# Kernel optimization log

Hardware: AMD Instinct MI355X
Metric: run time of the kernel (lower is better)

The kernel has to match this reference:

```python
import jax, jax.numpy as jnp
import numpy as np

N, L, D = 2, 1024, 4544
H, DKV = 71, 64
ROPE_BASE = 10000.0


def _rope_tables(seq_len, head_dim, dtype):
    inv_freq = 1.0 / (ROPE_BASE ** (jnp.arange(0, head_dim, 2, dtype=jnp.float32) / head_dim))
    t = jnp.arange(seq_len, dtype=jnp.float32)
    freqs = jnp.outer(t, inv_freq)               # [L, Dkv/2]
    emb = jnp.concatenate([freqs, freqs], -1)    # [L, Dkv]
    return jnp.cos(emb).astype(dtype), jnp.sin(emb).astype(dtype)


def _apply_rotary(x, cos, sin):
    # x: [..., L, Dkv]; cos/sin: [L, Dkv] broadcast
    left, right = jnp.split(x, 2, axis=-1)
    rotated = jnp.concatenate([-right, left], axis=-1)
    return x * cos + rotated * sin


def setup_inputs() -> dict:
    key = jax.random.key(0)
    k1, k2, k3 = jax.random.split(key, 3)
    hidden_states = jax.random.normal(k1, (N, L, D), dtype=jnp.float32)
    w_qkv = jax.random.normal(k2, (D + 2 * DKV, D), dtype=jnp.float32) * (1.0 / np.sqrt(D))
    w_dense = jax.random.normal(k3, (D, D), dtype=jnp.float32) * (1.0 / np.sqrt(D))
    return {"hidden_states": hidden_states, "w_qkv": w_qkv, "w_dense": w_dense}


def reference(hidden_states, w_qkv, w_dense):
    n, l, d = hidden_states.shape
    # fused QKV projection -> [N, L, H+2, Dkv]
    fused = (hidden_states @ w_qkv.T).reshape(n, l, H + 2, DKV)
    q = fused[:, :, :-2, :]          # [N, L, H, Dkv]
    k = fused[:, :, -2, :]           # [N, L, Dkv] (single MQA kv head)
    v = fused[:, :, -1, :]           # [N, L, Dkv]

    cos, sin = _rope_tables(l, DKV, hidden_states.dtype)
    q = _apply_rotary(q, cos[:, None, :], sin[:, None, :])   # broadcast over heads
    k = _apply_rotary(k, cos, sin)

    scale = 1.0 / np.sqrt(DKV)
    # scores: [N, H, Lq, Lk]; kv head broadcast across all H query heads
    scores = jnp.einsum('nqhd,nkd->nhqk', q, k) * scale
    causal = jnp.tril(jnp.ones((l, l), dtype=bool))
    scores = jnp.where(causal, scores, jnp.finfo(scores.dtype).min)
    attn = jax.nn.softmax(scores, axis=-1)
    out = jnp.einsum('nhqk,nkd->nqhd', attn, v)              # [N, L, H, Dkv]
    out = out.reshape(n, l, H * DKV)
    return out @ w_dense.T
```

## Files before the change

kernel.cpp:

```cpp
#include <hip/hip_runtime.h>

typedef unsigned short u16;
typedef __attribute__((ext_vector_type(8))) short short8;
typedef __attribute__((ext_vector_type(4))) float floatx4;

__device__ __forceinline__ u16 f2bf(float f) {
    union { float f; unsigned int u; } v;
    v.f = f;
    unsigned int u = v.u;
    return (u16)((u + 0x7FFFu + ((u >> 16) & 1u)) >> 16);
}

__device__ __forceinline__ void cvt8_f32_bf16(const float* __restrict__ p, u16* dst) {
    const float4 x = *(const float4*)p;
    const float4 y = *(const float4*)(p + 4);
    short8 s;
    s[0] = (short)f2bf(x.x); s[1] = (short)f2bf(x.y);
    s[2] = (short)f2bf(x.z); s[3] = (short)f2bf(x.w);
    s[4] = (short)f2bf(y.x); s[5] = (short)f2bf(y.y);
    s[6] = (short)f2bf(y.z); s[7] = (short)f2bf(y.w);
    *(short8*)dst = s;
}

__device__ __forceinline__ void gld_lds16(const u16* g, u16* l) {
    __builtin_amdgcn_global_load_lds(
        (const __attribute__((address_space(1))) void*)g,
        (__attribute__((address_space(3))) void*)l,
        16, 0, 0);
}

__global__ __launch_bounds__(256) void cvt3_kernel(
    const float* __restrict__ a, u16* __restrict__ oa, long na,
    const float* __restrict__ b, u16* __restrict__ ob, long nb,
    const float* __restrict__ c, u16* __restrict__ oc, long nc) {
    const float* in; u16* out; long n;
    if (blockIdx.y == 0)      { in = a; out = oa; n = na; }
    else if (blockIdx.y == 1) { in = b; out = ob; n = nb; }
    else                      { in = c; out = oc; n = nc; }
    const long i = ((long)blockIdx.x * 256 + threadIdx.x) * 8;
    if (i >= n) return;
    cvt8_f32_bf16(in + i, out + i);
}

__global__ __launch_bounds__(256) void gemm_qkv_bf(const u16* __restrict__ A,
                                                   const u16* __restrict__ B,
                                                   u16* __restrict__ qb,
                                                   u16* __restrict__ kb,
                                                   u16* __restrict__ vt,
                                                   int M, int N, int K) {
    __shared__ __align__(16) u16 a_lds[128 * 32];
    __shared__ __align__(16) u16 b_lds[128 * 32];
    const int t    = threadIdx.x;
    const int lane = t & 63;
    const int w    = t >> 6;
    const int quad = lane >> 4;
    const int l16  = lane & 15;
    const int m0 = blockIdx.y * 128;
    const int n0 = blockIdx.x * 128;
    const int wm = (w >> 1) * 64;
    const int wn = (w & 1) * 64;

    const int srow = t >> 2;
    const int scol = (t & 3) * 8;
    const u16* Ap0 = A + (long)(m0 + srow) * K + scol;
    const u16* Ap1 = A + (long)(m0 + 64 + srow) * K + scol;
    int bn0 = n0 + srow;      if (bn0 >= N) bn0 = N - 1;
    int bn1 = n0 + 64 + srow; if (bn1 >= N) bn1 = N - 1;
    const u16* Bp0 = B + (long)bn0 * K + scol;
    const u16* Bp1 = B + (long)bn1 * K + scol;

    u16* as0 = a_lds + srow * 32 + scol;
    u16* as1 = a_lds + (64 + srow) * 32 + scol;
    u16* bs0 = b_lds + srow * 32 + scol;
    u16* bs1 = b_lds + (64 + srow) * 32 + scol;

    floatx4 acc[4][4];
    const floatx4 zf4 = {0.f, 0.f, 0.f, 0.f};
#pragma unroll
    for (int i = 0; i < 4; i++)
#pragma unroll
        for (int j = 0; j < 4; j++) acc[i][j] = zf4;

    for (int k0 = 0; k0 < K; k0 += 32) {
        gld_lds16(Ap0 + k0, as0);
        gld_lds16(Ap1 + k0, as1);
        gld_lds16(Bp0 + k0, bs0);
        gld_lds16(Bp1 + k0, bs1);
        __syncthreads();
        short8 af[4], bfr[4];
#pragma unroll
        for (int i = 0; i < 4; i++)
            af[i] = *(const short8*)(a_lds + (wm + i * 16 + l16) * 32 + quad * 8);
#pragma unroll
        for (int j = 0; j < 4; j++)
            bfr[j] = *(const short8*)(b_lds + (wn + j * 16 + l16) * 32 + quad * 8);
#pragma unroll
        for (int i = 0; i < 4; i++)
#pragma unroll
            for (int j = 0; j < 4; j++)
                acc[i][j] = __builtin_amdgcn_mfma_f32_16x16x32_bf16(af[i], bfr[j], acc[i][j], 0, 0, 0);
        __syncthreads();
    }

#pragma unroll
    for (int j = 0; j < 4; j++) {
        const int c = n0 + wn + j * 16 + l16;
        if (c >= N) continue;
        const int hh = c >> 6;
        const int d  = c & 63;
        float inv = 0.f;
        if (hh < 72) inv = expf((float)(2 * (d & 31)) * (-0.14391156831212787f));
#pragma unroll
        for (int i = 0; i < 4; i++) {
#pragma unroll
            for (int r = 0; r < 4; r++) {
                const int row = m0 + wm + i * 16 + quad * 4 + r;
                const int tn = row >> 10;
                const int tl = row & 1023;
                float val = acc[i][j][r];
                if (hh < 72) {
                    float sv, cv;
                    sincosf((float)tl * inv, &sv, &cv);
                    const float pacc = acc[i][j ^ 2][r];
                    val = val * cv + ((d < 32) ? -pacc : pacc) * sv;
                }
                if (hh < 71) {
                    qb[((long)((tn * 71 + hh) * 1024 + tl)) * 64 + d] = f2bf(val * 0.125f);
                } else if (hh == 71) {
                    kb[((long)(tn * 1024 + tl)) * 64 + d] = f2bf(val);
                } else {
                    vt[((long)(tn * 64 + d)) * 1024 + tl] = f2bf(val);
                }
            }
        }
    }
}

__global__ __launch_bounds__(256) void gemm_dense_bf(const u16* __restrict__ A,
                                                     const u16* __restrict__ B,
                                                     float* __restrict__ C,
                                                     int M, int N, int K) {
    __shared__ __align__(16) u16 a_lds[128 * 32];
    __shared__ __align__(16) u16 b_lds[128 * 32];
    const int t    = threadIdx.x;
    const int lane = t & 63;
    const int w    = t >> 6;
    const int quad = lane >> 4;
    const int l16  = lane & 15;
    const int m0 = blockIdx.y * 128;
    const int n0 = blockIdx.x * 128;
    const int wm = (w >> 1) * 64;
    const int wn = (w & 1) * 64;

    const int srow = t >> 2;
    const int scol = (t & 3) * 8;
    const u16* Ap0 = A + (long)(m0 + srow) * K + scol;
    const u16* Ap1 = A + (long)(m0 + 64 + srow) * K + scol;
    int bn0 = n0 + srow;      if (bn0 >= N) bn0 = N - 1;
    int bn1 = n0 + 64 + srow; if (bn1 >= N) bn1 = N - 1;
    const u16* Bp0 = B + (long)bn0 * K + scol;
    const u16* Bp1 = B + (long)bn1 * K + scol;

    u16* as0 = a_lds + srow * 32 + scol;
    u16* as1 = a_lds + (64 + srow) * 32 + scol;
    u16* bs0 = b_lds + srow * 32 + scol;
    u16* bs1 = b_lds + (64 + srow) * 32 + scol;

    floatx4 acc[4][4];
    const floatx4 zf4 = {0.f, 0.f, 0.f, 0.f};
#pragma unroll
    for (int i = 0; i < 4; i++)
#pragma unroll
        for (int j = 0; j < 4; j++) acc[i][j] = zf4;

    for (int k0 = 0; k0 < K; k0 += 32) {
        gld_lds16(Ap0 + k0, as0);
        gld_lds16(Ap1 + k0, as1);
        gld_lds16(Bp0 + k0, bs0);
        gld_lds16(Bp1 + k0, bs1);
        __syncthreads();
        short8 af[4], bfr[4];
#pragma unroll
        for (int i = 0; i < 4; i++)
            af[i] = *(const short8*)(a_lds + (wm + i * 16 + l16) * 32 + quad * 8);
#pragma unroll
        for (int j = 0; j < 4; j++)
            bfr[j] = *(const short8*)(b_lds + (wn + j * 16 + l16) * 32 + quad * 8);
#pragma unroll
        for (int i = 0; i < 4; i++)
#pragma unroll
            for (int j = 0; j < 4; j++)
                acc[i][j] = __builtin_amdgcn_mfma_f32_16x16x32_bf16(af[i], bfr[j], acc[i][j], 0, 0, 0);
        __syncthreads();
    }

#pragma unroll
    for (int i = 0; i < 4; i++) {
#pragma unroll
        for (int j = 0; j < 4; j++) {
            const int col = n0 + wn + j * 16 + l16;
            if (col < N) {
#pragma unroll
                for (int r = 0; r < 4; r++) {
                    const int row = m0 + wm + i * 16 + quad * 4 + r;
                    C[(long)row * N + col] = acc[i][j][r];
                }
            }
        }
    }
}

__global__ __launch_bounds__(256) void attn_kernel2(const u16* __restrict__ qb,
                                                    const u16* __restrict__ kb,
                                                    const u16* __restrict__ vt,
                                                    u16* __restrict__ ao) {
    __shared__ __align__(16) u16 k_lds[2][64 * 72];
    __shared__ __align__(16) u16 v_lds[2][64 * 72];
    __shared__ __align__(16) u16 p_lds[4][16 * 72];
    const int qt2 = blockIdx.x;
    const int h   = blockIdx.y;
    const int n   = blockIdx.z;
    const int t    = threadIdx.x;
    const int w    = t >> 6;
    const int lane = t & 63;
    const int quad = lane >> 4;
    const int l16  = lane & 15;
    const int Q0 = qt2 * 128;

    short8 aq[2][2];
#pragma unroll
    for (int mf = 0; mf < 2; mf++) {
        const u16* qrow = qb +
            ((long)((n * 71 + h) * 1024 + Q0 + 64 * mf + w * 16 + l16)) * 64;
        aq[mf][0] = *(const short8*)(qrow + quad * 8);
        aq[mf][1] = *(const short8*)(qrow + 32 + quad * 8);
    }

    floatx4 o[2][4];
    float lst[2][4];
    const floatx4 zf4 = {0.f, 0.f, 0.f, 0.f};
#pragma unroll
    for (int mf = 0; mf < 2; mf++) {
#pragma unroll
        for (int i = 0; i < 4; i++) { o[mf][i] = zf4; lst[mf][i] = 0.f; }
    }

    const int srow = t >> 2;
    const int scol = (t & 3) * 16;
    const u16* kb_n = kb + (long)n * 1024 * 64;
    const u16* vt_n = vt + (long)n * 64 * 1024;
    u16* pw = p_lds[w];

    const int ktend = 2 * qt2 + 2;

    auto stage = [&](int kt, int b) {
        const u16* krow = kb_n + (long)(kt * 64 + srow) * 64 + scol;
        *(uint4*)(k_lds[b] + srow * 72 + scol)     = *(const uint4*)(krow);
        *(uint4*)(k_lds[b] + srow * 72 + scol + 8) = *(const uint4*)(krow + 8);
        const u16* vrow = vt_n + (long)srow * 1024 + kt * 64 + scol;
        *(uint4*)(v_lds[b] + srow * 72 + scol)     = *(const uint4*)(vrow);
        *(uint4*)(v_lds[b] + srow * 72 + scol + 8) = *(const uint4*)(vrow + 8);
    };

    stage(0, 0);
    for (int kt = 0; kt < ktend; kt++) {
        const int buf = kt & 1;
        __syncthreads();
        if (kt + 1 < ktend) stage(kt + 1, 1 - buf);

#pragma unroll
        for (int mf = 0; mf < 2; mf++) {
            if (mf == 0 && kt == 2 * qt2 + 1) continue;
            floatx4 s[4];
#pragma unroll
            for (int sub = 0; sub < 4; sub++) {
                const short8 b0 = *(const short8*)(k_lds[buf] + (sub * 16 + l16) * 72 + quad * 8);
                const short8 b1 = *(const short8*)(k_lds[buf] + (sub * 16 + l16) * 72 + 32 + quad * 8);
                floatx4 z = zf4;
                z = __builtin_amdgcn_mfma_f32_16x16x32_bf16(aq[mf][0], b0, z, 0, 0, 0);
                z = __builtin_amdgcn_mfma_f32_16x16x32_bf16(aq[mf][1], b1, z, 0, 0, 0);
                s[sub] = z;
            }
            const bool diag = (kt == 2 * qt2 + mf);
            const int rowb = Q0 + 64 * mf + w * 16 + quad * 4;
#pragma unroll
            for (int sub = 0; sub < 4; sub++) {
                const int key = kt * 64 + sub * 16 + l16;
#pragma unroll
                for (int r = 0; r < 4; r++) {
                    float p = __expf(s[sub][r]);
                    if (diag && key > rowb + r) p = 0.f;
                    lst[mf][r] += p;
                    pw[(quad * 4 + r) * 72 + sub * 16 + l16] = f2bf(p);
                }
            }
            const short8 ap0 = *(const short8*)(pw + l16 * 72 + quad * 8);
            const short8 ap1 = *(const short8*)(pw + l16 * 72 + 32 + quad * 8);
#pragma unroll
            for (int dch = 0; dch < 4; dch++) {
                const short8 bv0 = *(const short8*)(v_lds[buf] + (dch * 16 + l16) * 72 + quad * 8);
                const short8 bv1 = *(const short8*)(v_lds[buf] + (dch * 16 + l16) * 72 + 32 + quad * 8);
                o[mf][dch] = __builtin_amdgcn_mfma_f32_16x16x32_bf16(ap0, bv0, o[mf][dch], 0, 0, 0);
                o[mf][dch] = __builtin_amdgcn_mfma_f32_16x16x32_bf16(ap1, bv1, o[mf][dch], 0, 0, 0);
            }
        }
    }

    float lsum[2][4];
#pragma unroll
    for (int mf = 0; mf < 2; mf++) {
#pragma unroll
        for (int r = 0; r < 4; r++) {
            float v = lst[mf][r];
#pragma unroll
            for (int mk = 1; mk < 16; mk <<= 1) v += __shfl_xor(v, mk, 64);
            lsum[mf][r] = v;
        }
    }
#pragma unroll
    for (int mf = 0; mf < 2; mf++) {
#pragma unroll
        for (int dch = 0; dch < 4; dch++) {
#pragma unroll
            for (int r = 0; r < 4; r++) {
                const float val = o[mf][dch][r] / lsum[mf][r];
                const int row = n * 1024 + Q0 + 64 * mf + w * 16 + quad * 4 + r;
                const int col = h * 64 + dch * 16 + l16;
                ao[(long)row * 4544 + col] = f2bf(val);
            }
        }
    }
}

__global__ __launch_bounds__(256) void gemm_qkv_f32(const float* __restrict__ A,
                                                    const float* __restrict__ B,
                                                    u16* __restrict__ qb,
                                                    u16* __restrict__ kb,
                                                    u16* __restrict__ vt,
                                                    int M, int N, int K) {
    __shared__ __align__(16) u16 a_lds[128 * 32];
    __shared__ __align__(16) u16 b_lds[128 * 32];
    const int t    = threadIdx.x;
    const int lane = t & 63;
    const int w    = t >> 6;
    const int quad = lane >> 4;
    const int l16  = lane & 15;
    const int m0 = blockIdx.y * 128;
    const int n0 = blockIdx.x * 128;
    const int wm = (w >> 1) * 64;
    const int wn = (w & 1) * 64;
    const int srow = t >> 2;
    const int scol = (t & 3) * 8;
    const float* Ap0 = A + (long)(m0 + srow) * K + scol;
    const float* Ap1 = A + (long)(m0 + 64 + srow) * K + scol;
    int bn0 = n0 + srow;      if (bn0 >= N) bn0 = N - 1;
    int bn1 = n0 + 64 + srow; if (bn1 >= N) bn1 = N - 1;
    const float* Bp0 = B + (long)bn0 * K + scol;
    const float* Bp1 = B + (long)bn1 * K + scol;
    u16* as0 = a_lds + srow * 32 + scol;
    u16* as1 = a_lds + (64 + srow) * 32 + scol;
    u16* bs0 = b_lds + srow * 32 + scol;
    u16* bs1 = b_lds + (64 + srow) * 32 + scol;
    floatx4 acc[4][4];
    const floatx4 zf4 = {0.f, 0.f, 0.f, 0.f};
#pragma unroll
    for (int i = 0; i < 4; i++)
#pragma unroll
        for (int j = 0; j < 4; j++) acc[i][j] = zf4;
    for (int k0 = 0; k0 < K; k0 += 32) {
        cvt8_f32_bf16(Ap0 + k0, as0);
        cvt8_f32_bf16(Ap1 + k0, as1);
        cvt8_f32_bf16(Bp0 + k0, bs0);
        cvt8_f32_bf16(Bp1 + k0, bs1);
        __syncthreads();
        short8 af[4], bfr[4];
#pragma unroll
        for (int i = 0; i < 4; i++)
            af[i] = *(const short8*)(a_lds + (wm + i * 16 + l16) * 32 + quad * 8);
#pragma unroll
        for (int j = 0; j < 4; j++)
            bfr[j] = *(const short8*)(b_lds + (wn + j * 16 + l16) * 32 + quad * 8);
#pragma unroll
        for (int i = 0; i < 4; i++)
#pragma unroll
            for (int j = 0; j < 4; j++)
                acc[i][j] = __builtin_amdgcn_mfma_f32_16x16x32_bf16(af[i], bfr[j], acc[i][j], 0, 0, 0);
        __syncthreads();
    }
#pragma unroll
    for (int j = 0; j < 4; j++) {
        const int c = n0 + wn + j * 16 + l16;
        if (c >= N) continue;
        const int hh = c >> 6;
        const int d  = c & 63;
        float inv = 0.f;
        if (hh < 72) inv = expf((float)(2 * (d & 31)) * (-0.14391156831212787f));
#pragma unroll
        for (int i = 0; i < 4; i++) {
#pragma unroll
            for (int r = 0; r < 4; r++) {
                const int row = m0 + wm + i * 16 + quad * 4 + r;
                const int tn = row >> 10;
                const int tl = row & 1023;
                float val = acc[i][j][r];
                if (hh < 72) {
                    float sv, cv;
                    sincosf((float)tl * inv, &sv, &cv);
                    const float pacc = acc[i][j ^ 2][r];
                    val = val * cv + ((d < 32) ? -pacc : pacc) * sv;
                }
                if (hh < 71) {
                    qb[((long)((tn * 71 + hh) * 1024 + tl)) * 64 + d] = f2bf(val * 0.125f);
                } else if (hh == 71) {
                    kb[((long)(tn * 1024 + tl)) * 64 + d] = f2bf(val);
                } else {
                    vt[((long)(tn * 64 + d)) * 1024 + tl] = f2bf(val);
                }
            }
        }
    }
}

__global__ __launch_bounds__(256) void gemm_dense_f32(const u16* __restrict__ A,
                                                      const float* __restrict__ B,
                                                      float* __restrict__ C,
                                                      int M, int N, int K) {
    __shared__ __align__(16) u16 a_lds[128 * 32];
    __shared__ __align__(16) u16 b_lds[128 * 32];
    const int t    = threadIdx.x;
    const int lane = t & 63;
    const int w    = t >> 6;
    const int quad = lane >> 4;
    const int l16  = lane & 15;
    const int m0 = blockIdx.y * 128;
    const int n0 = blockIdx.x * 128;
    const int wm = (w >> 1) * 64;
    const int wn = (w & 1) * 64;
    const int srow = t >> 2;
    const int scol = (t & 3) * 8;
    const u16* Ap0 = A + (long)(m0 + srow) * K + scol;
    const u16* Ap1 = A + (long)(m0 + 64 + srow) * K + scol;
    int bn0 = n0 + srow;      if (bn0 >= N) bn0 = N - 1;
    int bn1 = n0 + 64 + srow; if (bn1 >= N) bn1 = N - 1;
    const float* Bp0 = B + (long)bn0 * K + scol;
    const float* Bp1 = B + (long)bn1 * K + scol;
    u16* as0 = a_lds + srow * 32 + scol;
    u16* as1 = a_lds + (64 + srow) * 32 + scol;
    u16* bs0 = b_lds + srow * 32 + scol;
    u16* bs1 = b_lds + (64 + srow) * 32 + scol;
    floatx4 acc[4][4];
    const floatx4 zf4 = {0.f, 0.f, 0.f, 0.f};
#pragma unroll
    for (int i = 0; i < 4; i++)
#pragma unroll
        for (int j = 0; j < 4; j++) acc[i][j] = zf4;
    for (int k0 = 0; k0 < K; k0 += 32) {
        *(uint4*)as0 = *(const uint4*)(Ap0 + k0);
        *(uint4*)as1 = *(const uint4*)(Ap1 + k0);
        cvt8_f32_bf16(Bp0 + k0, bs0);
        cvt8_f32_bf16(Bp1 + k0, bs1);
        __syncthreads();
        short8 af[4], bfr[4];
#pragma unroll
        for (int i = 0; i < 4; i++)
            af[i] = *(const short8*)(a_lds + (wm + i * 16 + l16) * 32 + quad * 8);
#pragma unroll
        for (int j = 0; j < 4; j++)
            bfr[j] = *(const short8*)(b_lds + (wn + j * 16 + l16) * 32 + quad * 8);
#pragma unroll
        for (int i = 0; i < 4; i++)
#pragma unroll
            for (int j = 0; j < 4; j++)
                acc[i][j] = __builtin_amdgcn_mfma_f32_16x16x32_bf16(af[i], bfr[j], acc[i][j], 0, 0, 0);
        __syncthreads();
    }
#pragma unroll
    for (int i = 0; i < 4; i++) {
#pragma unroll
        for (int j = 0; j < 4; j++) {
            const int col = n0 + wn + j * 16 + l16;
            if (col < N) {
#pragma unroll
                for (int r = 0; r < 4; r++) {
                    const int row = m0 + wm + i * 16 + quad * 4 + r;
                    C[(long)row * N + col] = acc[i][j][r];
                }
            }
        }
    }
}

extern "C" void kernel_launch(void* const* d_in, const int* in_sizes, int n_in,
                              void* d_out, int out_size, void* d_ws, size_t ws_size,
                              hipStream_t stream) {
    (void)in_sizes; (void)n_in; (void)out_size;
    const float* hidden  = (const float*)d_in[0];
    const float* w_qkv   = (const float*)d_in[1];
    const float* w_dense = (const float*)d_in[2];
    float* out = (float*)d_out;

    const long N_HID = (long)2048 * 4544;
    const long N_QKV = (long)4672 * 4544;
    const long N_DEN = (long)4544 * 4544;
    const long N_Q   = (long)2 * 71 * 1024 * 64;
    const long N_KV  = (long)2 * 1024 * 64;
    const long N_AO  = (long)2048 * 4544;

    const size_t needA = (size_t)(N_HID + N_QKV + N_DEN + N_Q + 2 * N_KV + N_AO) * 2;

    if (ws_size >= needA) {
        u16* hid_bf  = (u16*)d_ws;
        u16* wqkv_bf = hid_bf + N_HID;
        u16* wden_bf = wqkv_bf + N_QKV;
        u16* qbuf    = wden_bf + N_DEN;
        u16* kbuf    = qbuf + N_Q;
        u16* vtbuf   = kbuf + N_KV;
        u16* aout    = vtbuf + N_KV;

        cvt3_kernel<<<dim3(10366, 3), 256, 0, stream>>>(
            hidden, hid_bf, N_HID, w_qkv, wqkv_bf, N_QKV, w_dense, wden_bf, N_DEN);
        gemm_qkv_bf<<<dim3(37, 16), 256, 0, stream>>>(hid_bf, wqkv_bf,
                                                      qbuf, kbuf, vtbuf,
                                                      2048, 4672, 4544);
        attn_kernel2<<<dim3(8, 71, 2), 256, 0, stream>>>(qbuf, kbuf, vtbuf, aout);
        gemm_dense_bf<<<dim3(36, 16), 256, 0, stream>>>(aout, wden_bf, out,
                                                        2048, 4544, 4544);
    } else {
        u16* qbuf  = (u16*)d_ws;
        u16* kbuf  = qbuf + N_Q;
        u16* vtbuf = kbuf + N_KV;
        u16* aout  = vtbuf + N_KV;
        gemm_qkv_f32<<<dim3(37, 16), 256, 0, stream>>>(hidden, w_qkv,
                                                       qbuf, kbuf, vtbuf,
                                                       2048, 4672, 4544);
        attn_kernel2<<<dim3(8, 71, 2), 256, 0, stream>>>(qbuf, kbuf, vtbuf, aout);
        gemm_dense_f32<<<dim3(36, 16), 256, 0, stream>>>(aout, w_dense, out,
                                                         2048, 4544, 4544);
    }
}
```

Measured before the change: 616.5 us.

## Replace QKV and dense GEMMs with 256x256 8-wave pipelined double-buffered kernels

Both bf16 GEMMs move from 128x128 tiles with a single-buffered K=32 loop to 256x256 tiles run by 512 threads. Operands are double-buffered in LDS with K=64 steps and XOR-swizzled columns, and global-to-LDS loads are interleaved with MFMA phases using explicit barriers, waitcnt and setprio. Workgroup IDs are remapped across the 8 XCDs for cache locality. This aims to raise MFMA utilisation and hide load latency, at the cost of 128 KB of LDS per block and fewer blocks in the grid (152 and 144), which may leave some CUs idle.

```diff
diff --git a/kernel.cpp b/kernel.cpp
--- a/kernel.cpp
+++ b/kernel.cpp
@@ -42,86 +42,141 @@
     cvt8_f32_bf16(in + i, out + i);
 }
 
-__global__ __launch_bounds__(256) void gemm_qkv_bf(const u16* __restrict__ A,
-                                                   const u16* __restrict__ B,
-                                                   u16* __restrict__ qb,
-                                                   u16* __restrict__ kb,
-                                                   u16* __restrict__ vt,
-                                                   int M, int N, int K) {
-    __shared__ __align__(16) u16 a_lds[128 * 32];
-    __shared__ __align__(16) u16 b_lds[128 * 32];
-    const int t    = threadIdx.x;
-    const int lane = t & 63;
-    const int w    = t >> 6;
-    const int quad = lane >> 4;
-    const int l16  = lane & 15;
-    const int m0 = blockIdx.y * 128;
-    const int n0 = blockIdx.x * 128;
-    const int wm = (w >> 1) * 64;
-    const int wn = (w & 1) * 64;
-
-    const int srow = t >> 2;
-    const int scol = (t & 3) * 8;
-    const u16* Ap0 = A + (long)(m0 + srow) * K + scol;
-    const u16* Ap1 = A + (long)(m0 + 64 + srow) * K + scol;
-    int bn0 = n0 + srow;      if (bn0 >= N) bn0 = N - 1;
-    int bn1 = n0 + 64 + srow; if (bn1 >= N) bn1 = N - 1;
-    const u16* Bp0 = B + (long)bn0 * K + scol;
-    const u16* Bp1 = B + (long)bn1 * K + scol;
-
-    u16* as0 = a_lds + srow * 32 + scol;
-    u16* as1 = a_lds + (64 + srow) * 32 + scol;
-    u16* bs0 = b_lds + srow * 32 + scol;
-    u16* bs1 = b_lds + (64 + srow) * 32 + scol;
-
-    floatx4 acc[4][4];
-    const floatx4 zf4 = {0.f, 0.f, 0.f, 0.f};
-#pragma unroll
-    for (int i = 0; i < 4; i++)
-#pragma unroll
-        for (int j = 0; j < 4; j++) acc[i][j] = zf4;
-
-    for (int k0 = 0; k0 < K; k0 += 32) {
-        gld_lds16(Ap0 + k0, as0);
-        gld_lds16(Ap1 + k0, as1);
-        gld_lds16(Bp0 + k0, bs0);
-        gld_lds16(Bp1 + k0, bs1);
-        __syncthreads();
-        short8 af[4], bfr[4];
-#pragma unroll
-        for (int i = 0; i < 4; i++)
-            af[i] = *(const short8*)(a_lds + (wm + i * 16 + l16) * 32 + quad * 8);
-#pragma unroll
-        for (int j = 0; j < 4; j++)
-            bfr[j] = *(const short8*)(b_lds + (wn + j * 16 + l16) * 32 + quad * 8);
-#pragma unroll
-        for (int i = 0; i < 4; i++)
-#pragma unroll
-            for (int j = 0; j < 4; j++)
-                acc[i][j] = __builtin_amdgcn_mfma_f32_16x16x32_bf16(af[i], bfr[j], acc[i][j], 0, 0, 0);
-        __syncthreads();
-    }
-
-#pragma unroll
-    for (int j = 0; j < 4; j++) {
-        const int c = n0 + wn + j * 16 + l16;
+
+#define GEMM8P_PROLOGUE()                                                      \
+    const int t    = threadIdx.x;                                              \
+    const int w    = t >> 6;                                                   \
+    const int lane = t & 63;                                                   \
+    const int quad = lane >> 4;                                                \
+    const int l16  = lane & 15;                                                \
+    const int sw   = lane & 7;                                                 \
+    const int nwg  = gridDim.x;                                                \
+    const int qq = nwg >> 3, rr = nwg & 7;                                     \
+    const int xcd = blockIdx.x & 7, idx = blockIdx.x >> 3;                     \
+    const int wgid = (xcd < rr ? xcd * (qq + 1)                                \
+                               : rr * (qq + 1) + (xcd - rr) * qq) + idx;       \
+    const int m0 = (wgid / nt) * 256;                                          \
+    const int n0 = (wgid % nt) * 256;                                          \
+    const int wm = (w >> 2) * 128;                                             \
+    const int wn = (w & 3) * 64;                                               \
+    const int trow = t >> 3;                                                   \
+    const int scol = ((t & 7) ^ (trow & 7)) * 8;                               \
+    const long Kl = K;                                                         \
+    const u16* Asrc = A + (long)(m0 + trow) * Kl + scol;                       \
+    auto stageA = [&](int jt, int h, int b) {                                  \
+        _Pragma("unroll")                                                      \
+        for (int i = 0; i < 2; i++) {                                          \
+            const u16* src = Asrc + (long)(h * 128 + i * 64) * Kl + (long)jt * 64; \
+            u16* dst = &aLds[b][0] + h * 8192 + i * 4096 + t * 8;              \
+            gld_lds16(src, dst);                                               \
+        }                                                                      \
+    };                                                                         \
+    auto stageB = [&](int jt, int h, int b) {                                  \
+        _Pragma("unroll")                                                      \
+        for (int i = 0; i < 2; i++) {                                          \
+            int rb = n0 + h * 128 + i * 64 + trow;                             \
+            if (rb > N - 1) rb = N - 1;                                        \
+            const u16* src = B + (long)rb * Kl + scol + (long)jt * 64;         \
+            u16* dst = &bLds[b][0] + h * 8192 + i * 4096 + t * 8;              \
+            gld_lds16(src, dst);                                               \
+        }                                                                      \
+    };                                                                         \
+    floatx4 acc[8][4];                                                         \
+    const floatx4 zf4 = {0.f, 0.f, 0.f, 0.f};                                  \
+    _Pragma("unroll")                                                          \
+    for (int i = 0; i < 8; i++)                                                \
+        _Pragma("unroll")                                                      \
+        for (int j = 0; j < 4; j++) acc[i][j] = zf4;                           \
+                          \
+    stageA(0, 0, 0); stageA(0, 1, 0);                                          \
+    stageB(0, 0, 0); stageB(0, 1, 0);                                          \
+    stageB(1, 0, 1); stageB(1, 1, 1);                                          \
+    asm volatile("s_waitcnt vmcnt(4)" ::: "memory");                           \
+    __builtin_amdgcn_s_barrier();
+
+#define GPHASE(P, STAGE_STMT, TAIL_VM)                                         \
+    {                                                                          \
+        short8 afA[2], afB[2];                                                 \
+        _Pragma("unroll")                                                      \
+        for (int ks = 0; ks < 2; ks++) {                                       \
+            afA[ks] = *(const short8*)(Ac + (wm + (2 * (P)) * 16 + l16) * 64   \
+                                          + ((4 * ks + quad) ^ sw) * 8);       \
+            afB[ks] = *(const short8*)(Ac + (wm + (2 * (P) + 1) * 16 + l16) * 64 \
+                                          + ((4 * ks + quad) ^ sw) * 8);       \
+        }                                                                      \
+        STAGE_STMT;                                                            \
+        __builtin_amdgcn_s_barrier();                                          \
+        asm volatile("s_waitcnt lgkmcnt(0)" ::: "memory");                     \
+        __builtin_amdgcn_sched_barrier(0);                                     \
+        __builtin_amdgcn_s_setprio(1);                                         \
+        _Pragma("unroll")                                                      \
+        for (int ks = 0; ks < 2; ks++) {                                       \
+            _Pragma("unroll")                                                  \
+            for (int ni = 0; ni < 4; ni++) {                                   \
+                acc[2 * (P)][ni] = __builtin_amdgcn_mfma_f32_16x16x32_bf16(    \
+                    afA[ks], bf[ni][ks], acc[2 * (P)][ni], 0, 0, 0);           \
+                acc[2 * (P) + 1][ni] = __builtin_amdgcn_mfma_f32_16x16x32_bf16(\
+                    afB[ks], bf[ni][ks], acc[2 * (P) + 1][ni], 0, 0, 0);       \
+            }                                                                  \
+        }                                                                      \
+        __builtin_amdgcn_s_setprio(0);                                         \
+        TAIL_VM;                                                               \
+        __builtin_amdgcn_s_barrier();                                          \
+    }
+
+#define GEMM8P_KLOOP()                                                         \
+    const int JT = K >> 6;                                                     \
+    for (int j = 0; j < JT; ++j) {                                             \
+        const int cur = j & 1;                                                 \
+        const int nb  = cur ^ 1;                                               \
+        const int jn1 = (j + 1 < JT) ? j + 1 : JT - 1;                         \
+        const int jn2 = (j + 2 < JT) ? j + 2 : JT - 1;                         \
+        const u16* Ac = &aLds[cur][0];                                         \
+        const u16* Bc = &bLds[cur][0];                                         \
+        short8 bf[4][2];                                                       \
+        _Pragma("unroll")                                                      \
+        for (int ni = 0; ni < 4; ni++)                                         \
+            _Pragma("unroll")                                                  \
+            for (int ks = 0; ks < 2; ks++)                                     \
+                bf[ni][ks] = *(const short8*)(Bc + (wn + ni * 16 + l16) * 64   \
+                                                 + ((4 * ks + quad) ^ sw) * 8);\
+        GPHASE(0, stageA(jn1, 0, nb), );                                       \
+        GPHASE(1, stageA(jn1, 1, nb), );                                       \
+        GPHASE(2, stageB(jn2, 0, cur), );                                      \
+        GPHASE(3, stageB(jn2, 1, cur),                                         \
+               asm volatile("s_waitcnt vmcnt(4)" ::: "memory"));               \
+    }                                                                          \
+    asm volatile("s_waitcnt vmcnt(0)" ::: "memory");
+
+__global__ __launch_bounds__(512, 2) void gemm_qkv_8p(
+    const u16* __restrict__ A, const u16* __restrict__ B,
+    u16* __restrict__ qb, u16* __restrict__ kb, u16* __restrict__ vt,
+    int M, int N, int K, int nt) {
+    __shared__ __align__(16) u16 aLds[2][256 * 64];
+    __shared__ __align__(16) u16 bLds[2][256 * 64];
+    GEMM8P_PROLOGUE()
+    GEMM8P_KLOOP()
+
+#pragma unroll
+    for (int ni = 0; ni < 4; ni++) {
+        const int c = n0 + wn + ni * 16 + l16;
         if (c >= N) continue;
         const int hh = c >> 6;
         const int d  = c & 63;
         float inv = 0.f;
         if (hh < 72) inv = expf((float)(2 * (d & 31)) * (-0.14391156831212787f));
 #pragma unroll
-        for (int i = 0; i < 4; i++) {
+        for (int mi = 0; mi < 8; mi++) {
 #pragma unroll
             for (int r = 0; r < 4; r++) {
-                const int row = m0 + wm + i * 16 + quad * 4 + r;
+                const int row = m0 + wm + mi * 16 + quad * 4 + r;
                 const int tn = row >> 10;
                 const int tl = row & 1023;
-                float val = acc[i][j][r];
+                float val = acc[mi][ni][r];
                 if (hh < 72) {
                     float sv, cv;
                     sincosf((float)tl * inv, &sv, &cv);
-                    const float pacc = acc[i][j ^ 2][r];
+                    const float pacc = acc[mi][ni ^ 2][r];
                     val = val * cv + ((d < 32) ? -pacc : pacc) * sv;
                 }
                 if (hh < 71) {
@@ -136,75 +191,24 @@
     }
 }
 
-__global__ __launch_bounds__(256) void gemm_dense_bf(const u16* __restrict__ A,
-                                                     const u16* __restrict__ B,
-                                                     float* __restrict__ C,
-                                                     int M, int N, int K) {
-    __shared__ __align__(16) u16 a_lds[128 * 32];
-    __shared__ __align__(16) u16 b_lds[128 * 32];
-    const int t    = threadIdx.x;
-    const int lane = t & 63;
-    const int w    = t >> 6;
-    const int quad = lane >> 4;
-    const int l16  = lane & 15;
-    const int m0 = blockIdx.y * 128;
-    const int n0 = blockIdx.x * 128;
-    const int wm = (w >> 1) * 64;
-    const int wn = (w & 1) * 64;
-
-    const int srow = t >> 2;
-    const int scol = (t & 3) * 8;
-    const u16* Ap0 = A + (long)(m0 + srow) * K + scol;
-    const u16* Ap1 = A + (long)(m0 + 64 + srow) * K + scol;
-    int bn0 = n0 + srow;      if (bn0 >= N) bn0 = N - 1;
-    int bn1 = n0 + 64 + srow; if (bn1 >= N) bn1 = N - 1;
-    const u16* Bp0 = B + (long)bn0 * K + scol;
-    const u16* Bp1 = B + (long)bn1 * K + scol;
-
-    u16* as0 = a_lds + srow * 32 + scol;
-    u16* as1 = a_lds + (64 + srow) * 32 + scol;
-    u16* bs0 = b_lds + srow * 32 + scol;
-    u16* bs1 = b_lds + (64 + srow) * 32 + scol;
-
-    floatx4 acc[4][4];
-    const floatx4 zf4 = {0.f, 0.f, 0.f, 0.f};
-#pragma unroll
-    for (int i = 0; i < 4; i++)
-#pragma unroll
-        for (int j = 0; j < 4; j++) acc[i][j] = zf4;
-
-    for (int k0 = 0; k0 < K; k0 += 32) {
-        gld_lds16(Ap0 + k0, as0);
-        gld_lds16(Ap1 + k0, as1);
-        gld_lds16(Bp0 + k0, bs0);
-        gld_lds16(Bp1 + k0, bs1);
-        __syncthreads();
-        short8 af[4], bfr[4];
-#pragma unroll
-        for (int i = 0; i < 4; i++)
-            af[i] = *(const short8*)(a_lds + (wm + i * 16 + l16) * 32 + quad * 8);
-#pragma unroll
-        for (int j = 0; j < 4; j++)
-            bfr[j] = *(const short8*)(b_lds + (wn + j * 16 + l16) * 32 + quad * 8);
-#pragma unroll
-        for (int i = 0; i < 4; i++)
-#pragma unroll
-            for (int j = 0; j < 4; j++)
-                acc[i][j] = __builtin_amdgcn_mfma_f32_16x16x32_bf16(af[i], bfr[j], acc[i][j], 0, 0, 0);
-        __syncthreads();
-    }
-
-#pragma unroll
-    for (int i = 0; i < 4; i++) {
-#pragma unroll
-        for (int j = 0; j < 4; j++) {
-            const int col = n0 + wn + j * 16 + l16;
-            if (col < N) {
-#pragma unroll
-                for (int r = 0; r < 4; r++) {
-                    const int row = m0 + wm + i * 16 + quad * 4 + r;
-                    C[(long)row * N + col] = acc[i][j][r];
-                }
+__global__ __launch_bounds__(512, 2) void gemm_dense_8p(
+    const u16* __restrict__ A, const u16* __restrict__ B,
+    float* __restrict__ C, int M, int N, int K, int nt) {
+    __shared__ __align__(16) u16 aLds[2][256 * 64];
+    __shared__ __align__(16) u16 bLds[2][256 * 64];
+    GEMM8P_PROLOGUE()
+    GEMM8P_KLOOP()
+
+#pragma unroll
+    for (int ni = 0; ni < 4; ni++) {
+        const int col = n0 + wn + ni * 16 + l16;
+        if (col >= N) continue;
+#pragma unroll
+        for (int mi = 0; mi < 8; mi++) {
+#pragma unroll
+            for (int r = 0; r < 4; r++) {
+                const int row = m0 + wm + mi * 16 + quad * 4 + r;
+                C[(long)row * N + col] = acc[mi][ni][r];
             }
         }
     }
@@ -519,12 +523,12 @@
 
         cvt3_kernel<<<dim3(10366, 3), 256, 0, stream>>>(
             hidden, hid_bf, N_HID, w_qkv, wqkv_bf, N_QKV, w_dense, wden_bf, N_DEN);
-        gemm_qkv_bf<<<dim3(37, 16), 256, 0, stream>>>(hid_bf, wqkv_bf,
+        gemm_qkv_8p<<<dim3(8 * 19), 512, 0, stream>>>(hid_bf, wqkv_bf,
                                                       qbuf, kbuf, vtbuf,
-                                                      2048, 4672, 4544);
+                                                      2048, 4672, 4544, 19);
         attn_kernel2<<<dim3(8, 71, 2), 256, 0, stream>>>(qbuf, kbuf, vtbuf, aout);
-        gemm_dense_bf<<<dim3(36, 16), 256, 0, stream>>>(aout, wden_bf, out,
-                                                        2048, 4544, 4544);
+        gemm_dense_8p<<<dim3(8 * 18), 512, 0, stream>>>(aout, wden_bf, out,
+                                                        2048, 4544, 4544, 18);
     } else {
         u16* qbuf  = (u16*)d_ws;
         u16* kbuf  = qbuf + N_Q;
```

Result: no change. 622.9 us (+1.0%).
